# Optimization experiments

Hardware: AMD Instinct MI355X
Metric: run time of the kernel (lower is better)

## Reference

```python
import jax, jax.numpy as jnp
from jax import lax
import numpy as np

DN = ('NCHW', 'OIHW', 'NCHW')
EPS = 1e-8
LRELU_SLOPE = 0.2
SQRT2 = np.float32(np.sqrt(2.0))


def _blur2d(x):
    # 5x5 binomial FIR, depthwise, padding=2, stride=1 (Blur2d(kernel_size=5, padding=2))
    k1 = jnp.array([1.0, 4.0, 6.0, 4.0, 1.0], dtype=x.dtype)
    k2 = jnp.outer(k1, k1)
    k2 = k2 / k2.sum()
    C = x.shape[1]
    kern = jnp.broadcast_to(k2, (C, 1, 5, 5))
    return lax.conv_general_dilated(x, kern, window_strides=(1, 1),
                                    padding=[(2, 2), (2, 2)],
                                    feature_group_count=C,
                                    dimension_numbers=DN)


def _second_moment_norm(x, g):
    # normalize by per-channel spatial second moment, learnable gain g [C]
    ms = jnp.mean(jnp.square(x), axis=(2, 3), keepdims=True)  # [B,C,1,1]
    return x * lax.rsqrt(ms + EPS) * g[None, :, None, None]


def _modulated_conv(x, w, b, style_w, style_b, s, stride, padding):
    # StyleGAN2 modulated conv with demodulation, grouped-conv batch trick
    B, I, H, W = x.shape
    O, _, kh, kw = w.shape
    scale = np.float32(1.0 / np.sqrt(I * kh * kw))
    style = s @ style_w.T + style_b[None, :]                      # [B, I]
    wm = scale * w[None] * style[:, None, :, None, None]          # [B,O,I,kh,kw]
    d = lax.rsqrt(jnp.sum(jnp.square(wm), axis=(2, 3, 4)) + EPS)  # [B,O]
    wm = wm * d[:, :, None, None, None]
    xg = x.reshape(1, B * I, H, W)
    wg = wm.reshape(B * O, I, kh, kw)
    out = lax.conv_general_dilated(xg, wg, window_strides=(stride, stride),
                                   padding=[(padding, padding), (padding, padding)],
                                   feature_group_count=B,
                                   dimension_numbers=DN)
    out = out.reshape(B, O, out.shape[2], out.shape[3])
    return out + b[None, :, None, None]


def setup_inputs() -> dict:
    key = jax.random.key(0)
    ks = jax.random.split(key, 5)
    B, I, O, S, H, W, K = 8, 256, 256, 512, 128, 128, 3
    x = jax.random.normal(ks[0], (B, I, H, W), dtype=jnp.float32)
    s = jax.random.normal(ks[1], (B, S), dtype=jnp.float32)
    conv_w = jax.random.normal(ks[2], (O, I, K, K), dtype=jnp.float32)
    conv_b = jnp.zeros((O,), dtype=jnp.float32)
    style_w = jax.random.normal(ks[3], (I, S), dtype=jnp.float32) / np.float32(np.sqrt(S))
    style_b = jnp.ones((I,), dtype=jnp.float32)  # StyleGAN2 init: bias=1
    norm_g = jnp.ones((I,), dtype=jnp.float32)
    return {"x": x, "s": s, "conv_w": conv_w, "conv_b": conv_b,
            "style_w": style_w, "style_b": style_b, "norm_g": norm_g}


def reference(x, s, conv_w, conv_b, style_w, style_b, norm_g):
    x = _blur2d(x)                                   # blur (stride != 1 path)
    x = _second_moment_norm(x, norm_g)               # second-moment norm
    x = _modulated_conv(x, conv_w, conv_b, style_w, style_b, s, stride=2, padding=1)
    x = jnp.where(x >= 0, x, LRELU_SLOPE * x) * SQRT2  # scaled LeakyReLU
    return x
```

## Files before the change

### kernel.cpp

```cpp
#include <hip/hip_runtime.h>
#include <hip/hip_bf16.h>
#include <math.h>

#define B 8
#define IC 256
#define OC 256
#define SDIM 512
#define H 128
#define W 128
#define OH 64
#define OW 64
#define EPS 1e-8f
#define SQRT2 1.41421356237309504880f
#define SCALE 0.02083333395421505f

#define RS 16640
#define PLANE 1081600

typedef unsigned short u16;
typedef unsigned int u32;
typedef __attribute__((ext_vector_type(8))) short s16x8;
typedef __attribute__((ext_vector_type(4))) float f32x4;

__global__ void style_kernel(const float* __restrict__ s,
                             const float* __restrict__ sw,
                             const float* __restrict__ sb,
                             float* __restrict__ style) {
    int i = blockIdx.x * 256 + threadIdx.x;
    int b = i >> 8, ic = i & 255;
    const float* sv = s + (size_t)b * SDIM;
    const float* wv = sw + (size_t)ic * SDIM;
    float sum = 0.f;
    for (int k = 0; k < SDIM; ++k) sum = fmaf(sv[k], wv[k], sum);
    style[i] = sum + sb[ic];
}

__global__ void wsq_kernel(const float* __restrict__ w, float* __restrict__ wsq) {
    int i = blockIdx.x * 256 + threadIdx.x;
    const float* p = w + (size_t)i * 9;
    float sum = 0.f;
    for (int k = 0; k < 9; ++k) sum = fmaf(p[k], p[k], sum);
    wsq[i] = sum;
}

__global__ void demod_kernel(const float* __restrict__ style,
                             const float* __restrict__ wsq,
                             float* __restrict__ demod,
                             float* __restrict__ ssq) {
    int i = blockIdx.x * 256 + threadIdx.x;
    int b = i >> 8, o = i & 255;
    const float* st = style + b * 256;
    const float* wq = wsq + (size_t)o * 256;
    float sum = 0.f;
    for (int ic = 0; ic < 256; ++ic) {
        float sv = st[ic];
        sum = fmaf(sv * sv, wq[ic], sum);
    }
    demod[i] = rsqrtf(SCALE * SCALE * sum + EPS);
    ssq[i] = 0.f;
}

__global__ __launch_bounds__(256, 4) void blurpack_kernel(const float* __restrict__ x,
                                                          __hip_bfloat16* __restrict__ xbp,
                                                          float* __restrict__ ssq) {
    __shared__ u16 raw[8][12][128];
    __shared__ u16 pbuf[2][2][2][544];
    const int t = threadIdx.x;
    const int strip = blockIdx.x;
    const int ic0 = blockIdx.y << 3;
    const int b = blockIdx.z;

    #pragma unroll
    for (int k = 0; k < 6; ++k) {
        int sidx = t + (k << 8);
        int ch = sidx / 192;
        int rem = sidx - ch * 192;
        int r = rem >> 4, cg = rem & 15;
        int gr = (strip << 3) - 2 + r;
        uint4 q = {0u, 0u, 0u, 0u};
        if (gr >= 0 && gr < H) {
            const float* p = x + (((size_t)(b * 256 + ic0 + ch)) << 14) + (gr << 7) + (cg << 3);
            float4 v0 = *(const float4*)p;
            float4 v1 = *(const float4*)(p + 4);
            u16* qp = (u16*)&q;
            const float* vv0 = &v0.x;
            const float* vv1 = &v1.x;
            #pragma unroll
            for (int j = 0; j < 4; ++j) {
                __hip_bfloat16 b0 = __float2bfloat16(vv0[j]);
                __hip_bfloat16 b1 = __float2bfloat16(vv1[j]);
                qp[j] = *(u16*)&b0;
                qp[4 + j] = *(u16*)&b1;
            }
        }
        *(uint4*)&raw[ch][r][cg << 3] = q;
    }
    __syncthreads();

    const int hr = t >> 7;
    const int ch = (t >> 4) & 7;
    const int cg = t & 15;
    float ssacc = 0.f;

    for (int pass = 0; pass < 4; ++pass) {
        const int dp = pass & 1;
        const int br = (pass << 1) + hr;

        float f0[8], f1[8], f2[8], f3[8], f4[8];
        {
            uint4 q0 = *(const uint4*)&raw[ch][br + 0][cg << 3];
            uint4 q1 = *(const uint4*)&raw[ch][br + 1][cg << 3];
            uint4 q2 = *(const uint4*)&raw[ch][br + 2][cg << 3];
            uint4 q3 = *(const uint4*)&raw[ch][br + 3][cg << 3];
            uint4 q4 = *(const uint4*)&raw[ch][br + 4][cg << 3];
            const u16* h0 = (const u16*)&q0; const u16* h1 = (const u16*)&q1;
            const u16* h2 = (const u16*)&q2; const u16* h3 = (const u16*)&q3;
            const u16* h4 = (const u16*)&q4;
            #pragma unroll
            for (int j = 0; j < 8; ++j) {
                f0[j] = __uint_as_float(((u32)h0[j]) << 16);
                f1[j] = __uint_as_float(((u32)h1[j]) << 16);
                f2[j] = __uint_as_float(((u32)h2[j]) << 16);
                f3[j] = __uint_as_float(((u32)h3[j]) << 16);
                f4[j] = __uint_as_float(((u32)h4[j]) << 16);
            }
        }
        float v[8];
        #pragma unroll
        for (int j = 0; j < 8; ++j)
            v[j] = fmaf(6.f, f2[j], fmaf(4.f, f1[j] + f3[j], f0[j] + f4[j]));

        float vm2 = __shfl_up(v[6], 1, 64);
        float vm1 = __shfl_up(v[7], 1, 64);
        float vp1 = __shfl_down(v[0], 1, 64);
        float vp2 = __shfl_down(v[1], 1, 64);
        if (cg == 0)  { vm2 = 0.f; vm1 = 0.f; }
        if (cg == 15) { vp1 = 0.f; vp2 = 0.f; }
        float e[12];
        e[0] = vm2; e[1] = vm1;
        #pragma unroll
        for (int j = 0; j < 8; ++j) e[2 + j] = v[j];
        e[10] = vp1; e[11] = vp2;

        u16 hp[8];
        #pragma unroll
        for (int j = 0; j < 8; ++j) {
            float hv = fmaf(6.f, e[j + 2], fmaf(4.f, e[j + 1] + e[j + 3], e[j] + e[j + 4]))
                     * (1.0f / 256.0f);
            ssacc = fmaf(hv, hv, ssacc);
            __hip_bfloat16 hb = __float2bfloat16(hv);
            hp[j] = *(u16*)&hb;
        }
        u16 w0[4] = {hp[0], hp[2], hp[4], hp[6]};
        u16 w1[4] = {hp[1], hp[3], hp[5], hp[7]};
        *(uint2*)&pbuf[dp][hr][0][(ch << 6) + (cg << 2)] = *(const uint2*)w0;
        *(uint2*)&pbuf[dp][hr][1][(ch << 6) + (cg << 2)] = *(const uint2*)w1;
        __syncthreads();

        {
            int fc = t & 127;
            int hr2 = t >> 7;
            int pw = fc & 1, pcol = fc >> 1;
            uint4 g;
            u16* gp = (u16*)&g;
            #pragma unroll
            for (int c2 = 0; c2 < 8; ++c2)
                gp[c2] = pbuf[dp][hr2][pw][(c2 << 6) + pcol];
            size_t off = (size_t)((b << 2) + (hr2 << 1) + pw) * PLANE
                       + (size_t)((strip << 2) + pass + 1) * RS
                       + (size_t)(pcol + 1) * 256 + ic0;
            *(uint4*)(xbp + off) = g;
        }
    }

    float sv = ssacc;
    sv += __shfl_down(sv, 8, 16);
    sv += __shfl_down(sv, 4, 16);
    sv += __shfl_down(sv, 2, 16);
    sv += __shfl_down(sv, 1, 16);
    if (cg == 0) atomicAdd(&ssq[(b << 8) + ic0 + ch], sv);
}

__global__ void wf_kernel(const float* __restrict__ w,
                          const float* __restrict__ demod,
                          const float* __restrict__ ssq,
                          const float* __restrict__ style,
                          const float* __restrict__ g,
                          __hip_bfloat16* __restrict__ wf) {
    int bo = blockIdx.x;
    int b = bo >> 8, o = bo & 255;
    int ic = threadIdx.x;
    float fac = rsqrtf(ssq[(b << 8) + ic] * (1.0f / 16384.0f) + EPS)
              * g[ic] * style[(b << 8) + ic] * SCALE;
    float m = demod[bo] * fac;
    const float* wp = w + ((size_t)o * 256 + ic) * 9;
    __hip_bfloat16* dst = wf + (size_t)bo * 2304 + ic;
    #pragma unroll
    for (int t = 0; t < 9; ++t)
        dst[t * 256] = __float2bfloat16(wp[t] * m);
}

__global__ void zeropad_kernel(__hip_bfloat16* __restrict__ xbp) {
    int p = blockIdx.x;
    int t = threadIdx.x;
    char* base = (char*)(xbp + (size_t)p * PLANE);
    uint4 z = {0u, 0u, 0u, 0u};
    for (int k = 0; k < 9; ++k) {
        int c = t + (k << 8);
        if (c < 2080) *(uint4*)(base + (size_t)c * 16) = z;
    }
    for (int k = 0; k < 8; ++k) {
        int c = t + (k << 8);
        int r = 1 + (c >> 5);
        int off = (c & 31) << 3;
        *(uint4*)(base + ((size_t)r * RS + off) * 2) = z;
    }
}

__device__ __forceinline__ void gl_lds16(const void* g, void* l) {
    __builtin_amdgcn_global_load_lds((const __attribute__((address_space(1))) u32*)g,
                                     (__attribute__((address_space(3))) u32*)l, 16, 0, 0);
}

__global__ __launch_bounds__(256, 2) void conv_kernel(const __hip_bfloat16* __restrict__ xbp,
                                                      const __hip_bfloat16* __restrict__ wf,
                                                      const float* __restrict__ bias,
                                                      float* __restrict__ out) {
    __shared__ char lds[16384];
    const int t = threadIdx.x;
    const int o0 = blockIdx.x << 7;
    const int n0 = blockIdx.y << 7;
    const int b  = blockIdx.z;
    const size_t bb = (size_t)b << 8;

    const int mA  = t >> 2;
    const int kgl = t & 3;
    const int kga = kgl ^ ((mA >> 1) & 3);
    size_t preA0 = (bb + o0 + mA) * 2304 + (kga << 3);
    size_t preA1 = preA0 + (size_t)64 * 2304;
    const int ow = mA & 63;
    size_t preB0 = (size_t)(blockIdx.y << 1) * RS + (size_t)ow * 256 + (kga << 3);
    size_t preB1 = preB0 + RS;
    char* dA0 = lds + t * 16;
    char* dA1 = lds + 4096 + t * 16;
    char* dB0 = lds + 8192 + t * 16;
    char* dB1 = lds + 12288 + t * 16;

    const int lane = t & 63, wave = t >> 6;
    const int lr = lane & 15, quad = lane >> 4;
    const int mb = (wave & 1) << 6;
    const int nb = (wave >> 1) << 6;
    const int fragoff = ((quad ^ ((lr >> 1) & 3)) << 4);

    f32x4 acc[4][4];
    #pragma unroll
    for (int i = 0; i < 4; ++i)
        #pragma unroll
        for (int j = 0; j < 4; ++j) acc[i][j] = (f32x4){0.f, 0.f, 0.f, 0.f};

    for (int kk = 0; kk < 72; ++kk) {
        int tap = kk >> 3;
        int ic0 = (kk & 7) << 5;
        int th = (tap * 11) >> 5;
        int tw = tap - th * 3;
        int ph  = (th == 1) ? 0 : 1;
        int dhp = (th == 0) ? 0 : 1;
        int pw  = (tw == 1) ? 0 : 1;
        int dwp = (tw == 0) ? 0 : 1;
        size_t boff = (size_t)((b << 2) + (ph << 1) + pw) * PLANE
                    + (size_t)dhp * RS + (dwp << 8) + ic0;
        size_t aoff = (size_t)kk << 5;

        __syncthreads();
        gl_lds16(wf + preA0 + aoff, dA0);
        gl_lds16(wf + preA1 + aoff, dA1);
        gl_lds16(xbp + preB0 + boff, dB0);
        gl_lds16(xbp + preB1 + boff, dB1);
        __syncthreads();

        s16x8 a[4], bf[4];
        #pragma unroll
        for (int i = 0; i < 4; ++i)
            a[i] = *(const s16x8*)(lds + ((mb + (i << 4) + lr) << 6) + fragoff);
        #pragma unroll
        for (int j = 0; j < 4; ++j)
            bf[j] = *(const s16x8*)(lds + 8192 + ((nb + (j << 4) + lr) << 6) + fragoff);
        #pragma unroll
        for (int i = 0; i < 4; ++i)
            #pragma unroll
            for (int j = 0; j < 4; ++j)
                acc[i][j] = __builtin_amdgcn_mfma_f32_16x16x32_bf16(a[i], bf[j], acc[i][j], 0, 0, 0);
    }

    float bi[4][4];
    #pragma unroll
    for (int i = 0; i < 4; ++i)
        #pragma unroll
        for (int rr = 0; rr < 4; ++rr)
            bi[i][rr] = bias[o0 + mb + (i << 4) + (quad << 2) + rr];
    #pragma unroll
    for (int i = 0; i < 4; ++i) {
        #pragma unroll
        for (int j = 0; j < 4; ++j) {
            #pragma unroll
            for (int rr = 0; rr < 4; ++rr) {
                int oc = o0 + mb + (i << 4) + (quad << 2) + rr;
                int n = n0 + nb + (j << 4) + lr;
                int oh = n >> 6, ow2 = n & 63;
                float v = acc[i][j][rr] + bi[i][rr];
                v = (v >= 0.f ? v : 0.2f * v) * SQRT2;
                out[((bb + oc) << 12) + (oh << 6) + ow2] = v;
            }
        }
    }
}

extern "C" void kernel_launch(void* const* d_in, const int* in_sizes, int n_in,
                              void* d_out, int out_size, void* d_ws, size_t ws_size,
                              hipStream_t stream) {
    const float* x   = (const float*)d_in[0];
    const float* s   = (const float*)d_in[1];
    const float* cw  = (const float*)d_in[2];
    const float* cb  = (const float*)d_in[3];
    const float* sw  = (const float*)d_in[4];
    const float* sb  = (const float*)d_in[5];
    const float* ng  = (const float*)d_in[6];
    float* out = (float*)d_out;

    char* ws = (char*)d_ws;
    __hip_bfloat16* xbp = (__hip_bfloat16*)ws;
    __hip_bfloat16* wfb = (__hip_bfloat16*)(ws + 69222400);
    float* style  = (float*)(ws + 78659584);
    float* wsq    = style + 2048;
    float* demod  = wsq + 65536;
    float* ssq    = demod + 2048;

    style_kernel<<<8, 256, 0, stream>>>(s, sw, sb, style);
    wsq_kernel<<<256, 256, 0, stream>>>(cw, wsq);
    demod_kernel<<<8, 256, 0, stream>>>(style, wsq, demod, ssq);
    blurpack_kernel<<<dim3(16, 32, 8), 256, 0, stream>>>(x, xbp, ssq);
    wf_kernel<<<2048, 256, 0, stream>>>(cw, demod, ssq, style, ng, wfb);
    zeropad_kernel<<<32, 256, 0, stream>>>(xbp);
    conv_kernel<<<dim3(2, 32, 8), 256, 0, stream>>>(xbp, wfb, cb, out);
}
```

Before: 336.8 us.

## Deepen conv K-chunk, shrink blur strips, fuse style/demod and zero-pad kernels

The conv kernel now stages 128-wide K chunks (64KB LDS) per barrier pair instead of 32-wide ones, cutting the loop from 72 to 18 iterations with an XOR-swizzled layout. This is meant to reduce sync and load-issue overhead per MFMA, at the cost of lower occupancy. The blur kernel processes 4-row strips with twice as many blocks and a higher launch-bounds occupancy target. The style and demod kernels are fused into one, and the zero-pad work is folded into the wf kernel, removing two launches.

```diff
diff --git a/kernel.cpp b/kernel.cpp
--- a/kernel.cpp
+++ b/kernel.cpp
@@ -22,19 +22,6 @@
 typedef __attribute__((ext_vector_type(8))) short s16x8;
 typedef __attribute__((ext_vector_type(4))) float f32x4;
 
-__global__ void style_kernel(const float* __restrict__ s,
-                             const float* __restrict__ sw,
-                             const float* __restrict__ sb,
-                             float* __restrict__ style) {
-    int i = blockIdx.x * 256 + threadIdx.x;
-    int b = i >> 8, ic = i & 255;
-    const float* sv = s + (size_t)b * SDIM;
-    const float* wv = sw + (size_t)ic * SDIM;
-    float sum = 0.f;
-    for (int k = 0; k < SDIM; ++k) sum = fmaf(sv[k], wv[k], sum);
-    style[i] = sum + sb[ic];
-}
-
 __global__ void wsq_kernel(const float* __restrict__ w, float* __restrict__ wsq) {
     int i = blockIdx.x * 256 + threadIdx.x;
     const float* p = w + (size_t)i * 9;
@@ -43,27 +30,44 @@
     wsq[i] = sum;
 }
 
-__global__ void demod_kernel(const float* __restrict__ style,
-                             const float* __restrict__ wsq,
-                             float* __restrict__ demod,
-                             float* __restrict__ ssq) {
-    int i = blockIdx.x * 256 + threadIdx.x;
-    int b = i >> 8, o = i & 255;
-    const float* st = style + b * 256;
-    const float* wq = wsq + (size_t)o * 256;
+__global__ __launch_bounds__(256) void style_demod_kernel(const float* __restrict__ s,
+                                                          const float* __restrict__ sw,
+                                                          const float* __restrict__ sb,
+                                                          const float* __restrict__ wsq,
+                                                          float* __restrict__ style,
+                                                          float* __restrict__ demod,
+                                                          float* __restrict__ ssq) {
+    __shared__ float st[256];
+    const int b = blockIdx.x;
+    const int tid = threadIdx.x;
+    const float4* sv = (const float4*)(s + (size_t)b * SDIM);
+    const float4* wv = (const float4*)(sw + (size_t)tid * SDIM);
     float sum = 0.f;
-    for (int ic = 0; ic < 256; ++ic) {
-        float sv = st[ic];
-        sum = fmaf(sv * sv, wq[ic], sum);
-    }
-    demod[i] = rsqrtf(SCALE * SCALE * sum + EPS);
-    ssq[i] = 0.f;
-}
-
-__global__ __launch_bounds__(256, 4) void blurpack_kernel(const float* __restrict__ x,
+    #pragma unroll 4
+    for (int k = 0; k < 128; ++k) {
+        float4 a4 = sv[k], b4 = wv[k];
+        sum = fmaf(a4.x, b4.x, fmaf(a4.y, b4.y, fmaf(a4.z, b4.z, fmaf(a4.w, b4.w, sum))));
+    }
+    float styv = sum + sb[tid];
+    style[(b << 8) + tid] = styv;
+    st[tid] = styv;
+    ssq[(b << 8) + tid] = 0.f;
+    __syncthreads();
+    const float4* wq = (const float4*)(wsq + (size_t)tid * 256);
+    float acc = 0.f;
+    #pragma unroll 4
+    for (int k = 0; k < 64; ++k) {
+        float4 q = wq[k];
+        float s0 = st[4 * k], s1 = st[4 * k + 1], s2 = st[4 * k + 2], s3 = st[4 * k + 3];
+        acc = fmaf(s0 * s0, q.x, fmaf(s1 * s1, q.y, fmaf(s2 * s2, q.z, fmaf(s3 * s3, q.w, acc))));
+    }
+    demod[(b << 8) + tid] = rsqrtf(SCALE * SCALE * acc + EPS);
+}
+
+__global__ __launch_bounds__(256, 6) void blurpack_kernel(const float* __restrict__ x,
                                                           __hip_bfloat16* __restrict__ xbp,
                                                           float* __restrict__ ssq) {
-    __shared__ u16 raw[8][12][128];
+    __shared__ u16 raw[8][8][128];
     __shared__ u16 pbuf[2][2][2][544];
     const int t = threadIdx.x;
     const int strip = blockIdx.x;
@@ -71,12 +75,12 @@
     const int b = blockIdx.z;
 
     #pragma unroll
-    for (int k = 0; k < 6; ++k) {
+    for (int k = 0; k < 4; ++k) {
         int sidx = t + (k << 8);
-        int ch = sidx / 192;
-        int rem = sidx - ch * 192;
+        int ch = sidx >> 7;
+        int rem = sidx & 127;
         int r = rem >> 4, cg = rem & 15;
-        int gr = (strip << 3) - 2 + r;
+        int gr = (strip << 2) - 2 + r;
         uint4 q = {0u, 0u, 0u, 0u};
         if (gr >= 0 && gr < H) {
             const float* p = x + (((size_t)(b * 256 + ic0 + ch)) << 14) + (gr << 7) + (cg << 3);
@@ -102,11 +106,11 @@
     const int cg = t & 15;
     float ssacc = 0.f;
 
-    for (int pass = 0; pass < 4; ++pass) {
-        const int dp = pass & 1;
+    #pragma unroll
+    for (int pass = 0; pass < 2; ++pass) {
         const int br = (pass << 1) + hr;
 
-        float f0[8], f1[8], f2[8], f3[8], f4[8];
+        float v[8];
         {
             uint4 q0 = *(const uint4*)&raw[ch][br + 0][cg << 3];
             uint4 q1 = *(const uint4*)&raw[ch][br + 1][cg << 3];
@@ -118,17 +122,14 @@
             const u16* h4 = (const u16*)&q4;
             #pragma unroll
             for (int j = 0; j < 8; ++j) {
-                f0[j] = __uint_as_float(((u32)h0[j]) << 16);
-                f1[j] = __uint_as_float(((u32)h1[j]) << 16);
-                f2[j] = __uint_as_float(((u32)h2[j]) << 16);
-                f3[j] = __uint_as_float(((u32)h3[j]) << 16);
-                f4[j] = __uint_as_float(((u32)h4[j]) << 16);
+                float f0 = __uint_as_float(((u32)h0[j]) << 16);
+                float f1 = __uint_as_float(((u32)h1[j]) << 16);
+                float f2 = __uint_as_float(((u32)h2[j]) << 16);
+                float f3 = __uint_as_float(((u32)h3[j]) << 16);
+                float f4 = __uint_as_float(((u32)h4[j]) << 16);
+                v[j] = fmaf(6.f, f2, fmaf(4.f, f1 + f3, f0 + f4));
             }
         }
-        float v[8];
-        #pragma unroll
-        for (int j = 0; j < 8; ++j)
-            v[j] = fmaf(6.f, f2[j], fmaf(4.f, f1[j] + f3[j], f0[j] + f4[j]));
 
         float vm2 = __shfl_up(v[6], 1, 64);
         float vm1 = __shfl_up(v[7], 1, 64);
@@ -153,8 +154,8 @@
         }
         u16 w0[4] = {hp[0], hp[2], hp[4], hp[6]};
         u16 w1[4] = {hp[1], hp[3], hp[5], hp[7]};
-        *(uint2*)&pbuf[dp][hr][0][(ch << 6) + (cg << 2)] = *(const uint2*)w0;
-        *(uint2*)&pbuf[dp][hr][1][(ch << 6) + (cg << 2)] = *(const uint2*)w1;
+        *(uint2*)&pbuf[pass][hr][0][(ch << 6) + (cg << 2)] = *(const uint2*)w0;
+        *(uint2*)&pbuf[pass][hr][1][(ch << 6) + (cg << 2)] = *(const uint2*)w1;
         __syncthreads();
 
         {
@@ -165,20 +166,20 @@
             u16* gp = (u16*)&g;
             #pragma unroll
             for (int c2 = 0; c2 < 8; ++c2)
-                gp[c2] = pbuf[dp][hr2][pw][(c2 << 6) + pcol];
+                gp[c2] = pbuf[pass][hr2][pw][(c2 << 6) + pcol];
             size_t off = (size_t)((b << 2) + (hr2 << 1) + pw) * PLANE
-                       + (size_t)((strip << 2) + pass + 1) * RS
+                       + (size_t)((strip << 1) + pass + 1) * RS
                        + (size_t)(pcol + 1) * 256 + ic0;
             *(uint4*)(xbp + off) = g;
         }
     }
 
-    float sv = ssacc;
-    sv += __shfl_down(sv, 8, 16);
-    sv += __shfl_down(sv, 4, 16);
-    sv += __shfl_down(sv, 2, 16);
-    sv += __shfl_down(sv, 1, 16);
-    if (cg == 0) atomicAdd(&ssq[(b << 8) + ic0 + ch], sv);
+    float sv2 = ssacc;
+    sv2 += __shfl_down(sv2, 8, 16);
+    sv2 += __shfl_down(sv2, 4, 16);
+    sv2 += __shfl_down(sv2, 2, 16);
+    sv2 += __shfl_down(sv2, 1, 16);
+    if (cg == 0) atomicAdd(&ssq[(b << 8) + ic0 + ch], sv2);
 }
 
 __global__ void wf_kernel(const float* __restrict__ w,
@@ -186,7 +187,8 @@
                           const float* __restrict__ ssq,
                           const float* __restrict__ style,
                           const float* __restrict__ g,
-                          __hip_bfloat16* __restrict__ wf) {
+                          __hip_bfloat16* __restrict__ wf,
+                          __hip_bfloat16* __restrict__ xbp) {
     int bo = blockIdx.x;
     int b = bo >> 8, o = bo & 255;
     int ic = threadIdx.x;
@@ -198,22 +200,21 @@
     #pragma unroll
     for (int t = 0; t < 9; ++t)
         dst[t * 256] = __float2bfloat16(wp[t] * m);
-}
-
-__global__ void zeropad_kernel(__hip_bfloat16* __restrict__ xbp) {
-    int p = blockIdx.x;
-    int t = threadIdx.x;
-    char* base = (char*)(xbp + (size_t)p * PLANE);
-    uint4 z = {0u, 0u, 0u, 0u};
-    for (int k = 0; k < 9; ++k) {
-        int c = t + (k << 8);
-        if (c < 2080) *(uint4*)(base + (size_t)c * 16) = z;
-    }
-    for (int k = 0; k < 8; ++k) {
-        int c = t + (k << 8);
-        int r = 1 + (c >> 5);
-        int off = (c & 31) << 3;
-        *(uint4*)(base + ((size_t)r * RS + off) * 2) = z;
+
+    if (bo < 32) {
+        int t = threadIdx.x;
+        char* base = (char*)(xbp + (size_t)bo * PLANE);
+        uint4 z = {0u, 0u, 0u, 0u};
+        for (int k = 0; k < 9; ++k) {
+            int c = t + (k << 8);
+            if (c < 2080) *(uint4*)(base + (size_t)c * 16) = z;
+        }
+        for (int k = 0; k < 8; ++k) {
+            int c = t + (k << 8);
+            int r = 1 + (c >> 5);
+            int off = (c & 31) << 3;
+            *(uint4*)(base + ((size_t)r * RS + off) * 2) = z;
+        }
     }
 }
 
@@ -226,31 +227,32 @@
                                                       const __hip_bfloat16* __restrict__ wf,
                                                       const float* __restrict__ bias,
                                                       float* __restrict__ out) {
-    __shared__ char lds[16384];
+    __shared__ char lds[65536];
     const int t = threadIdx.x;
     const int o0 = blockIdx.x << 7;
-    const int n0 = blockIdx.y << 7;
+    const int y  = blockIdx.y;
     const int b  = blockIdx.z;
     const size_t bb = (size_t)b << 8;
 
-    const int mA  = t >> 2;
-    const int kgl = t & 3;
-    const int kga = kgl ^ ((mA >> 1) & 3);
-    size_t preA0 = (bb + o0 + mA) * 2304 + (kga << 3);
-    size_t preA1 = preA0 + (size_t)64 * 2304;
-    const int ow = mA & 63;
-    size_t preB0 = (size_t)(blockIdx.y << 1) * RS + (size_t)ow * 256 + (kga << 3);
-    size_t preB1 = preB0 + RS;
-    char* dA0 = lds + t * 16;
-    char* dA1 = lds + 4096 + t * 16;
-    char* dB0 = lds + 8192 + t * 16;
-    char* dB1 = lds + 12288 + t * 16;
+    u32 aoffs[8], boffs[8];
+    #pragma unroll
+    for (int j = 0; j < 8; ++j) {
+        int s = t + (j << 8);
+        int r = s >> 4, m = s & 15;
+        int g = m ^ (r & 7);
+        aoffs[j] = (u32)(r * 2304 + (g << 3)) * 2;
+        boffs[j] = (u32)((((y << 1) + (r >> 6)) * RS) + ((r & 63) << 8) + (g << 3)) * 2;
+    }
+    char* ldsA = lds;
+    char* ldsB = lds + 32768;
+    char* dstA = ldsA + t * 16;
+    char* dstB = ldsB + t * 16;
+    const char* gAbase = (const char*)(wf + (bb + o0) * 2304);
 
     const int lane = t & 63, wave = t >> 6;
     const int lr = lane & 15, quad = lane >> 4;
     const int mb = (wave & 1) << 6;
     const int nb = (wave >> 1) << 6;
-    const int fragoff = ((quad ^ ((lr >> 1) & 3)) << 4);
 
     f32x4 acc[4][4];
     #pragma unroll
@@ -258,38 +260,41 @@
         #pragma unroll
         for (int j = 0; j < 4; ++j) acc[i][j] = (f32x4){0.f, 0.f, 0.f, 0.f};
 
-    for (int kk = 0; kk < 72; ++kk) {
-        int tap = kk >> 3;
-        int ic0 = (kk & 7) << 5;
+    for (int c = 0; c < 18; ++c) {
+        int tap = c >> 1;
+        int ich = (c & 1) << 7;
         int th = (tap * 11) >> 5;
         int tw = tap - th * 3;
         int ph  = (th == 1) ? 0 : 1;
         int dhp = (th == 0) ? 0 : 1;
         int pw  = (tw == 1) ? 0 : 1;
         int dwp = (tw == 0) ? 0 : 1;
-        size_t boff = (size_t)((b << 2) + (ph << 1) + pw) * PLANE
-                    + (size_t)dhp * RS + (dwp << 8) + ic0;
-        size_t aoff = (size_t)kk << 5;
-
+        const char* gA = gAbase + (size_t)(tap * 256 + ich) * 2;
+        const char* gB = (const char*)(xbp + (size_t)((b << 2) + (ph << 1) + pw) * PLANE
+                                       + (size_t)dhp * RS + (dwp << 8) + ich);
         __syncthreads();
-        gl_lds16(wf + preA0 + aoff, dA0);
-        gl_lds16(wf + preA1 + aoff, dA1);
-        gl_lds16(xbp + preB0 + boff, dB0);
-        gl_lds16(xbp + preB1 + boff, dB1);
+        #pragma unroll
+        for (int j = 0; j < 8; ++j) gl_lds16(gA + aoffs[j], dstA + (j << 12));
+        #pragma unroll
+        for (int j = 0; j < 8; ++j) gl_lds16(gB + boffs[j], dstB + (j << 12));
         __syncthreads();
 
-        s16x8 a[4], bf[4];
-        #pragma unroll
-        for (int i = 0; i < 4; ++i)
-            a[i] = *(const s16x8*)(lds + ((mb + (i << 4) + lr) << 6) + fragoff);
-        #pragma unroll
-        for (int j = 0; j < 4; ++j)
-            bf[j] = *(const s16x8*)(lds + 8192 + ((nb + (j << 4) + lr) << 6) + fragoff);
-        #pragma unroll
-        for (int i = 0; i < 4; ++i)
+        #pragma unroll
+        for (int s = 0; s < 4; ++s) {
+            const int mq = ((s << 2) + quad) ^ (lr & 7);
+            s16x8 a[4], bf[4];
+            #pragma unroll
+            for (int i = 0; i < 4; ++i)
+                a[i] = *(const s16x8*)(ldsA + ((mb + (i << 4) + lr) << 8) + (mq << 4));
             #pragma unroll
             for (int j = 0; j < 4; ++j)
-                acc[i][j] = __builtin_amdgcn_mfma_f32_16x16x32_bf16(a[i], bf[j], acc[i][j], 0, 0, 0);
+                bf[j] = *(const s16x8*)(ldsB + ((nb + (j << 4) + lr) << 8) + (mq << 4));
+            #pragma unroll
+            for (int i = 0; i < 4; ++i)
+                #pragma unroll
+                for (int j = 0; j < 4; ++j)
+                    acc[i][j] = __builtin_amdgcn_mfma_f32_16x16x32_bf16(a[i], bf[j], acc[i][j], 0, 0, 0);
+        }
     }
 
     float bi[4][4];
@@ -298,6 +303,7 @@
         #pragma unroll
         for (int rr = 0; rr < 4; ++rr)
             bi[i][rr] = bias[o0 + mb + (i << 4) + (quad << 2) + rr];
+    const int n0 = y << 7;
     #pragma unroll
     for (int i = 0; i < 4; ++i) {
         #pragma unroll
@@ -335,11 +341,9 @@
     float* demod  = wsq + 65536;
     float* ssq    = demod + 2048;
 
-    style_kernel<<<8, 256, 0, stream>>>(s, sw, sb, style);
     wsq_kernel<<<256, 256, 0, stream>>>(cw, wsq);
-    demod_kernel<<<8, 256, 0, stream>>>(style, wsq, demod, ssq);
-    blurpack_kernel<<<dim3(16, 32, 8), 256, 0, stream>>>(x, xbp, ssq);
-    wf_kernel<<<2048, 256, 0, stream>>>(cw, demod, ssq, style, ng, wfb);
-    zeropad_kernel<<<32, 256, 0, stream>>>(xbp);
+    style_demod_kernel<<<8, 256, 0, stream>>>(s, sw, sb, wsq, style, demod, ssq);
+    blurpack_kernel<<<dim3(32, 32, 8), 256, 0, stream>>>(x, xbp, ssq);
+    wf_kernel<<<2048, 256, 0, stream>>>(cw, demod, ssq, style, ng, wfb, xbp);
     conv_kernel<<<dim3(2, 32, 8), 256, 0, stream>>>(xbp, wfb, cb, out);
 }
```

New measurement: 322.8 us. 4.2% less time.
